# Kernel tuning notes

Hardware: AMD Instinct MI355X
Metric: run time of the kernel (lower is better)

## Reference

```python
import jax, jax.numpy as jnp
import numpy as np

MARGIN = 0.1
NUM_BINS = 1600  # FastAP histogram bins over squared-distance range [0, 4]


def _fastap_rewards(x, labels):
    """Per-query FastAP (Cakir et al.) with soft (triangular) histogram binning.
    x: [n, d] L2-normalized embeddings; labels: [n] int. Returns [n] rewards.
    Uses the fact that a triangular pulse of width delta spreads each distance
    over exactly two adjacent bins -> scatter-add instead of an [n,n,L] tensor."""
    n = x.shape[0]
    L = NUM_BINS + 1
    delta = 4.0 / NUM_BINS
    dist2 = jnp.clip(2.0 - 2.0 * (x @ x.T), 0.0, 4.0)  # [n, n]
    same = labels[:, None] == labels[None, :]
    eye = jnp.eye(n, dtype=bool)
    i_pos = same & ~eye
    i_neg = ~same

    t = dist2 / delta
    idx0 = jnp.clip(jnp.floor(t).astype(jnp.int32), 0, L - 1)
    idx1 = jnp.clip(idx0 + 1, 0, L - 1)
    frac = t - jnp.floor(t)
    rows = jnp.broadcast_to(jnp.arange(n)[:, None], (n, n))

    def hist(mask):
        m = mask.astype(x.dtype)
        h = jnp.zeros((n, L), x.dtype)
        h = h.at[rows, idx0].add((1.0 - frac) * m)
        h = h.at[rows, idx1].add(frac * m)
        return h

    h_pos = hist(i_pos)
    h_neg = hist(i_neg)
    H_pos = jnp.cumsum(h_pos, axis=1)
    H_all = jnp.cumsum(h_pos + h_neg, axis=1)
    n_pos = jnp.sum(i_pos, axis=1).astype(x.dtype)
    safe = H_all > 0
    ap = jnp.sum(jnp.where(safe, h_pos * H_pos / jnp.where(safe, H_all, 1.0), 0.0), axis=1)
    return jnp.where(n_pos > 0, ap / jnp.maximum(n_pos, 1.0), 0.0)


def _per_row_loss(inputs_col, targets_col, inputs_row, targets_row):
    """Vectorized form of compute_loss_list. Sorting in the original only serves
    to extract max pos / max neg similarity, so per-row maxima + masked sums
    reproduce the exact same math."""
    n = inputs_col.shape[0]
    sim = inputs_col @ inputs_row.T  # [n, m]
    pos = targets_col[:, None] == targets_row[None, :]
    neg = ~pos  # computed BEFORE removing the diagonal, as in the original
    eye = jnp.eye(n, dtype=bool)
    pos = pos.at[:, :n].set(pos[:, :n] & ~eye)

    has_pos = jnp.any(pos, axis=1)
    neg_max = jnp.max(jnp.where(neg, sim, -jnp.inf), axis=1)  # neg_pair_[-1]
    pos_max = jnp.max(jnp.where(pos, sim, -jnp.inf), axis=1)  # pos_pair_[-1]

    pos_sel = pos & (sim < (neg_max + MARGIN)[:, None])
    pos_loss = jnp.sum(jnp.where(pos_sel, 1.0 - sim, 0.0), axis=1)

    thr = jnp.maximum(0.6, pos_max) - MARGIN
    neg_sel = neg & (sim > thr[:, None])
    neg_loss = jnp.sum(jnp.where(neg_sel, sim, 0.0), axis=1)

    return jnp.where(has_pos, pos_loss + neg_loss, 0.0), n


def setup_inputs() -> dict:
    key = jax.random.key(0)
    k1, k2, k3, k4, k5 = jax.random.split(key, 5)
    n, m, d, ncls = 4096, 4096, 128, 512

    def unit(k, shape):
        v = jax.random.normal(k, shape, dtype=jnp.float32)
        return v / jnp.linalg.norm(v, axis=-1, keepdims=True)

    return {
        "inputs_col": unit(k1, (n, d)),
        "targets_col": jax.random.randint(k2, (n,), 0, ncls),
        "inputs_row": unit(k3, (m, d)),
        "targets_row": jax.random.randint(k4, (m,), 0, ncls),
        "reward_labels": jax.random.randint(k5, (n,), 0, ncls),
    }


def reference(inputs_col, targets_col, inputs_row, targets_row, reward_labels):
    loss_i, n = _per_row_loss(inputs_col, targets_col, inputs_row, targets_row)
    # torch.tensor(rewards) detaches rewards from the graph -> stop_gradient
    rewards = jax.lax.stop_gradient(_fastap_rewards(inputs_col, reward_labels))
    return jnp.sum(loss_i * (1.0 - rewards)) / n
```

## Files before the change

kernel.cpp:

```cpp
#include <hip/hip_runtime.h>


#define N_ROWS 4096
#define DIM 128
#define TILE 128
#define L_BINS 1601

typedef __bf16 bf16x8 __attribute__((ext_vector_type(8)));
typedef float f32x4 __attribute__((ext_vector_type(4)));

__device__ __forceinline__ unsigned short f32_to_bf16(float f) {
    unsigned int u = __float_as_uint(f);
    u = (u + 0x7FFFu + ((u >> 16) & 1u)) >> 16;
    return (unsigned short)u;
}

__device__ __forceinline__ float bf16_lo(unsigned int u) {
    return __uint_as_float(u << 16);
}
__device__ __forceinline__ float bf16_hi(unsigned int u) {
    return __uint_as_float(u & 0xFFFF0000u);
}

__device__ __forceinline__ void unpack8(uint4 pk, float* s) {
    s[0] = bf16_lo(pk.x); s[1] = bf16_hi(pk.x);
    s[2] = bf16_lo(pk.y); s[3] = bf16_hi(pk.y);
    s[4] = bf16_lo(pk.z); s[5] = bf16_hi(pk.z);
    s[6] = bf16_lo(pk.w); s[7] = bf16_hi(pk.w);
}

__device__ __forceinline__ void async_copy16(const void* g, void* l) {
    __builtin_amdgcn_global_load_lds(
        (const __attribute__((address_space(1))) unsigned int*)g,
        (__attribute__((address_space(3))) unsigned int*)l, 16, 0, 0);
}

__global__ __launch_bounds__(256) void cvt2_kernel(const float4* __restrict__ a,
                                                   const float4* __restrict__ b,
                                                   ushort4* __restrict__ oa,
                                                   ushort4* __restrict__ ob,
                                                   int nvec) {
    for (int idx = blockIdx.x * 256 + threadIdx.x; idx < 2 * nvec; idx += gridDim.x * 256) {
        bool second = idx >= nvec;
        int k = second ? idx - nvec : idx;
        float4 v = second ? b[k] : a[k];
        ushort4 o;
        o.x = f32_to_bf16(v.x); o.y = f32_to_bf16(v.y);
        o.z = f32_to_bf16(v.z); o.w = f32_to_bf16(v.w);
        if (second) ob[k] = o; else oa[k] = o;
    }
}

__global__ __launch_bounds__(256) void gemm_tile_kernel(const unsigned short* __restrict__ A,
                                                        const unsigned short* __restrict__ B0,
                                                        const unsigned short* __restrict__ B1,
                                                        unsigned short* __restrict__ C0,
                                                        unsigned short* __restrict__ C1,
                                                        int N) {
    __shared__ unsigned short As[TILE * DIM];
    __shared__ unsigned short Bs[TILE * DIM];
    int w = threadIdx.x >> 6;
    int lane = threadIdx.x & 63;
    int tm = blockIdx.y, tn = blockIdx.x;
    const unsigned short* B = blockIdx.z ? B1 : B0;
    unsigned short* C = blockIdx.z ? C1 : C0;

    const char* ga = (const char*)(A + (size_t)tm * TILE * DIM);
    const char* gb = (const char*)(B + (size_t)tn * TILE * DIM);
#pragma unroll
    for (int it = 0; it < 8; ++it) {
        int off = (w * 8 + it) * 1024;
        async_copy16(ga + off + lane * 16, (char*)As + off);
        async_copy16(gb + off + lane * 16, (char*)Bs + off);
    }
    __syncthreads();

    int wm = (w & 1) * 64;
    int wn = (w >> 1) * 64;
    int quad = lane >> 4;
    int l15 = lane & 15;

    f32x4 acc[4][4] = {};
#pragma unroll
    for (int kk = 0; kk < 4; ++kk) {
        int kb = kk * 32 + quad * 8;
        bf16x8 af[4], bfr[4];
#pragma unroll
        for (int mi = 0; mi < 4; ++mi)
            af[mi] = *(const bf16x8*)&As[(wm + mi * 16 + l15) * DIM + kb];
#pragma unroll
        for (int ni = 0; ni < 4; ++ni)
            bfr[ni] = *(const bf16x8*)&Bs[(wn + ni * 16 + l15) * DIM + kb];
#pragma unroll
        for (int mi = 0; mi < 4; ++mi)
#pragma unroll
            for (int ni = 0; ni < 4; ++ni)
                acc[mi][ni] = __builtin_amdgcn_mfma_f32_16x16x32_bf16(af[mi], bfr[ni], acc[mi][ni], 0, 0, 0);
    }

#pragma unroll
    for (int mi = 0; mi < 4; ++mi) {
        int row0 = tm * TILE + wm + mi * 16 + quad * 4;
#pragma unroll
        for (int ni = 0; ni < 4; ++ni) {
            int col = tn * TILE + wn + ni * 16 + l15;
#pragma unroll
            for (int r = 0; r < 4; ++r)
                C[(size_t)(row0 + r) * N + col] = f32_to_bf16(acc[mi][ni][r]);
        }
    }
}

__global__ __launch_bounds__(256) void loss_kernel(const unsigned short* __restrict__ sim,
                                                   const int* __restrict__ tcol,
                                                   const int* __restrict__ trow,
                                                   float* __restrict__ loss,
                                                   int n, int m) {
    int i = (blockIdx.x * 256 + threadIdx.x) >> 6;
    int lane = threadIdx.x & 63;
    int myt = tcol[i];

    const uint4* simv = (const uint4*)(sim + (size_t)i * m);
    const int4* labv = (const int4*)trow;

    uint4 pk[8];
    unsigned long long posm = 0ull, negm = 0ull;
    float pmax = -3e38f, nmax = -3e38f;
#pragma unroll
    for (int v = 0; v < 8; ++v) {
        int vi = v * 64 + lane;
        pk[v] = simv[vi];
        int4 l0 = labv[2 * vi];
        int4 l1 = labv[2 * vi + 1];
        int j0 = vi * 8;
        float s[8];
        unpack8(pk[v], s);
        int lab[8] = {l0.x, l0.y, l0.z, l0.w, l1.x, l1.y, l1.z, l1.w};
#pragma unroll
        for (int k = 0; k < 8; ++k) {
            int j = j0 + k;
            bool same = (lab[k] == myt);
            bool posf = same && (j != i);
            if (posf) pmax = fmaxf(pmax, s[k]);
            if (!same) nmax = fmaxf(nmax, s[k]);
            posm |= ((unsigned long long)posf) << (v * 8 + k);
            negm |= ((unsigned long long)(!same)) << (v * 8 + k);
        }
    }
#pragma unroll
    for (int off = 32; off > 0; off >>= 1) {
        pmax = fmaxf(pmax, __shfl_xor(pmax, off));
        nmax = fmaxf(nmax, __shfl_xor(nmax, off));
    }

    float thr_n = nmax + 0.1f;
    float thr_p = fmaxf(0.6f, pmax) - 0.1f;
    float pl = 0.f, nl = 0.f;
#pragma unroll
    for (int v = 0; v < 8; ++v) {
        float s[8];
        unpack8(pk[v], s);
#pragma unroll
        for (int k = 0; k < 8; ++k) {
            int bit = v * 8 + k;
            bool posf = (posm >> bit) & 1ull;
            bool negf = (negm >> bit) & 1ull;
            pl += (posf && s[k] < thr_n) ? 1.f - s[k] : 0.f;
            nl += (negf && s[k] > thr_p) ? s[k] : 0.f;
        }
    }
    float tot = pl + nl;
#pragma unroll
    for (int off = 32; off > 0; off >>= 1) tot += __shfl_xor(tot, off);
    if (lane == 0) loss[i] = (pmax > -1e30f) ? tot : 0.f;
}

__global__ __launch_bounds__(256) void fastap_kernel(const unsigned short* __restrict__ gram,
                                                     const int* __restrict__ labels,
                                                     float* __restrict__ reward,
                                                     int n) {
    __shared__ unsigned long long hist[L_BINS];
    __shared__ unsigned long long wsum[4];
    __shared__ float apw[4];
    __shared__ int npw[4];
    int i = blockIdx.x;
    int t = threadIdx.x;
    int w = t >> 6;
    int lane = t & 63;

    for (int b = t; b < L_BINS; b += 256) hist[b] = 0ull;
    __syncthreads();

    int li = labels[i];
    int npos = 0;
    const uint4* gv = (const uint4*)(gram + (size_t)i * n);
    const int4* labv = (const int4*)labels;

    for (int v = t; v < (n >> 3); v += 256) {
        uint4 pk = gv[v];
        int4 l0 = labv[2 * v];
        int4 l1 = labv[2 * v + 1];
        int j0 = v << 3;
        float s[8];
        unpack8(pk, s);
        int lab[8] = {l0.x, l0.y, l0.z, l0.w, l1.x, l1.y, l1.z, l1.w};
#pragma unroll
        for (int k = 0; k < 8; ++k) {
            int j = j0 + k;
            float d2 = fminf(fmaxf(2.f - 2.f * s[k], 0.f), 4.f);
            float tt = d2 * 400.0f;
            float fl = floorf(tt);
            int i0 = (int)fl;
            if (i0 > L_BINS - 1) i0 = L_BINS - 1;
            int i1 = i0 + 1;
            if (i1 > L_BINS - 1) i1 = L_BINS - 1;
            unsigned int w1 = (unsigned int)((tt - fl) * 65536.0f);
            unsigned int w0 = 65536u - w1;
            bool diag = (j == i);
            if (diag) { w0 = 0u; w1 = 0u; }
            bool posf = (lab[k] == li) && !diag;
            unsigned long long hi = posf ? 1ull : 0ull;
            atomicAdd(&hist[i0], (unsigned long long)w0 | ((hi * w0) << 32));
            atomicAdd(&hist[i1], (unsigned long long)w1 | ((hi * w1) << 32));
            npos += posf ? 1 : 0;
        }
    }
    __syncthreads();

    const int CH = 7;
    int base = t * CH;
    unsigned long long lc[CH];
    unsigned long long run = 0ull;
#pragma unroll
    for (int k = 0; k < CH; ++k) {
        int idx = base + k;
        unsigned long long h = (idx < L_BINS) ? hist[idx] : 0ull;
        run += h;
        lc[k] = run;
    }
    unsigned long long tsum = run;
    unsigned long long sc = tsum;
#pragma unroll
    for (int off = 1; off < 64; off <<= 1) {
        unsigned long long v2 = __shfl_up(sc, off);
        if (lane >= off) sc += v2;
    }
    if (lane == 63) wsum[w] = sc;
    __syncthreads();
    unsigned long long woff = 0ull;
    for (int ww = 0; ww < w; ++ww) woff += wsum[ww];
    unsigned long long throff = woff + sc - tsum;

    float ap = 0.f;
#pragma unroll
    for (int k = 0; k < CH; ++k) {
        int idx = base + k;
        if (idx < L_BINS) {
            unsigned long long h = hist[idx];
            unsigned int hp = (unsigned int)(h >> 32);
            if (hp) {
                unsigned long long cum = lc[k] + throff;
                unsigned int Hp = (unsigned int)(cum >> 32);
                unsigned int Ha = (unsigned int)cum;
                ap += (float)hp * (float)Hp / (float)Ha;
            }
        }
    }
#pragma unroll
    for (int off = 32; off > 0; off >>= 1) {
        ap += __shfl_xor(ap, off);
        npos += __shfl_xor(npos, off);
    }
    if (lane == 0) { apw[w] = ap; npw[w] = npos; }
    __syncthreads();
    if (t == 0) {
        float A = apw[0] + apw[1] + apw[2] + apw[3];
        int np = npw[0] + npw[1] + npw[2] + npw[3];
        reward[i] = (np > 0) ? A * (1.0f / 65536.0f) / (float)np : 0.f;
    }
}

__global__ __launch_bounds__(256) void final_kernel(const float* __restrict__ loss,
                                                    const float* __restrict__ reward,
                                                    float* __restrict__ out, int n) {
    __shared__ float r[256];
    int t = threadIdx.x;
    float s = 0.f;
    for (int j = t; j < n; j += 256) s += loss[j] * (1.f - reward[j]);
    r[t] = s;
    __syncthreads();
    for (int off = 128; off > 0; off >>= 1) {
        if (t < off) r[t] += r[t + off];
        __syncthreads();
    }
    if (t == 0) out[0] = r[0] / (float)n;
}

extern "C" void kernel_launch(void* const* d_in, const int* in_sizes, int n_in,
                              void* d_out, int out_size, void* d_ws, size_t ws_size,
                              hipStream_t stream) {
    const float* inputs_col = (const float*)d_in[0];
    const int* targets_col = (const int*)d_in[1];
    const float* inputs_row = (const float*)d_in[2];
    const int* targets_row = (const int*)d_in[3];
    const int* reward_labels = (const int*)d_in[4];
    float* out = (float*)d_out;

    const int n = N_ROWS, m = N_ROWS, d = DIM;
    char* ws = (char*)d_ws;
    const size_t MB = 1048576;
    unsigned short* simbuf = (unsigned short*)ws;
    unsigned short* grambuf = (unsigned short*)(ws + 32 * MB);
    unsigned short* Abf = (unsigned short*)(ws + 64 * MB);
    unsigned short* Rbf = (unsigned short*)(ws + 65 * MB);
    float* loss = (float*)(ws + 66 * MB);
    float* reward = loss + n;

    cvt2_kernel<<<512, 256, 0, stream>>>((const float4*)inputs_col, (const float4*)inputs_row,
                                         (ushort4*)Abf, (ushort4*)Rbf, n * d / 4);

    dim3 ggrid(n / TILE, n / TILE, 2);
    gemm_tile_kernel<<<ggrid, 256, 0, stream>>>(Abf, Rbf, Abf, simbuf, grambuf, m);

    loss_kernel<<<n / 4, 256, 0, stream>>>(simbuf, targets_col, targets_row, loss, n, m);

    fastap_kernel<<<n, 256, 0, stream>>>(grambuf, reward_labels, reward, n);

    final_kernel<<<1, 256, 0, stream>>>(loss, reward, out, n);
}
```

Before: 136.4 us.

## Fuse per-row loss and FastAP histogram kernels into one block-per-row kernel

```diff
diff --git a/kernel.cpp b/kernel.cpp
--- a/kernel.cpp
+++ b/kernel.cpp
@@ -111,102 +111,76 @@
     }
 }
 
-__global__ __launch_bounds__(256) void loss_kernel(const unsigned short* __restrict__ sim,
-                                                   const int* __restrict__ tcol,
-                                                   const int* __restrict__ trow,
-                                                   float* __restrict__ loss,
-                                                   int n, int m) {
-    int i = (blockIdx.x * 256 + threadIdx.x) >> 6;
-    int lane = threadIdx.x & 63;
+__global__ __launch_bounds__(256) void lossap_kernel(const unsigned short* __restrict__ sim,
+                                                     const unsigned short* __restrict__ gram,
+                                                     const int* __restrict__ tcol,
+                                                     const int* __restrict__ trow,
+                                                     const int* __restrict__ rlab,
+                                                     float* __restrict__ contrib,
+                                                     int n) {
+    __shared__ unsigned long long hist[L_BINS];
+    __shared__ unsigned long long wsum[4];
+    __shared__ float pmx[4], nmx[4], lsum[4], apw[4];
+    __shared__ int npw[4];
+    int i = blockIdx.x;
+    int t = threadIdx.x;
+    int w = t >> 6, lane = t & 63;
+
+    for (int b = t; b < L_BINS; b += 256) hist[b] = 0ull;
+
     int myt = tcol[i];
-
-    const uint4* simv = (const uint4*)(sim + (size_t)i * m);
-    const int4* labv = (const int4*)trow;
-
-    uint4 pk[8];
-    unsigned long long posm = 0ull, negm = 0ull;
+    int li = rlab[i];
+    const uint4* simv = (const uint4*)(sim + (size_t)i * n);
+    const uint4* grav = (const uint4*)(gram + (size_t)i * n);
+    const int4* trv = (const int4*)trow;
+    const int4* rlv = (const int4*)rlab;
+
+    uint4 spk[2], gpk[2];
+    int4 tl[4], rl[4];
+#pragma unroll
+    for (int vv = 0; vv < 2; ++vv) {
+        int vi = vv * 256 + t;
+        spk[vv] = simv[vi];
+        gpk[vv] = grav[vi];
+        tl[2 * vv] = trv[2 * vi];
+        tl[2 * vv + 1] = trv[2 * vi + 1];
+        rl[2 * vv] = rlv[2 * vi];
+        rl[2 * vv + 1] = rlv[2 * vi + 1];
+    }
+
     float pmax = -3e38f, nmax = -3e38f;
-#pragma unroll
-    for (int v = 0; v < 8; ++v) {
-        int vi = v * 64 + lane;
-        pk[v] = simv[vi];
-        int4 l0 = labv[2 * vi];
-        int4 l1 = labv[2 * vi + 1];
-        int j0 = vi * 8;
+    unsigned int posm = 0, negm = 0;
+#pragma unroll
+    for (int vv = 0; vv < 2; ++vv) {
+        int vi = vv * 256 + t;
         float s[8];
-        unpack8(pk[v], s);
-        int lab[8] = {l0.x, l0.y, l0.z, l0.w, l1.x, l1.y, l1.z, l1.w};
+        unpack8(spk[vv], s);
+        int lab[8] = {tl[2 * vv].x, tl[2 * vv].y, tl[2 * vv].z, tl[2 * vv].w,
+                      tl[2 * vv + 1].x, tl[2 * vv + 1].y, tl[2 * vv + 1].z, tl[2 * vv + 1].w};
 #pragma unroll
         for (int k = 0; k < 8; ++k) {
-            int j = j0 + k;
+            int j = vi * 8 + k;
             bool same = (lab[k] == myt);
             bool posf = same && (j != i);
             if (posf) pmax = fmaxf(pmax, s[k]);
             if (!same) nmax = fmaxf(nmax, s[k]);
-            posm |= ((unsigned long long)posf) << (v * 8 + k);
-            negm |= ((unsigned long long)(!same)) << (v * 8 + k);
-        }
-    }
-#pragma unroll
-    for (int off = 32; off > 0; off >>= 1) {
-        pmax = fmaxf(pmax, __shfl_xor(pmax, off));
-        nmax = fmaxf(nmax, __shfl_xor(nmax, off));
-    }
-
-    float thr_n = nmax + 0.1f;
-    float thr_p = fmaxf(0.6f, pmax) - 0.1f;
-    float pl = 0.f, nl = 0.f;
-#pragma unroll
-    for (int v = 0; v < 8; ++v) {
+            posm |= ((unsigned int)posf) << (vv * 8 + k);
+            negm |= ((unsigned int)(!same)) << (vv * 8 + k);
+        }
+    }
+    __syncthreads();
+
+    int npos = 0;
+#pragma unroll
+    for (int vv = 0; vv < 2; ++vv) {
+        int vi = vv * 256 + t;
         float s[8];
-        unpack8(pk[v], s);
+        unpack8(gpk[vv], s);
+        int lab[8] = {rl[2 * vv].x, rl[2 * vv].y, rl[2 * vv].z, rl[2 * vv].w,
+                      rl[2 * vv + 1].x, rl[2 * vv + 1].y, rl[2 * vv + 1].z, rl[2 * vv + 1].w};
 #pragma unroll
         for (int k = 0; k < 8; ++k) {
-            int bit = v * 8 + k;
-            bool posf = (posm >> bit) & 1ull;
-            bool negf = (negm >> bit) & 1ull;
-            pl += (posf && s[k] < thr_n) ? 1.f - s[k] : 0.f;
-            nl += (negf && s[k] > thr_p) ? s[k] : 0.f;
-        }
-    }
-    float tot = pl + nl;
-#pragma unroll
-    for (int off = 32; off > 0; off >>= 1) tot += __shfl_xor(tot, off);
-    if (lane == 0) loss[i] = (pmax > -1e30f) ? tot : 0.f;
-}
-
-__global__ __launch_bounds__(256) void fastap_kernel(const unsigned short* __restrict__ gram,
-                                                     const int* __restrict__ labels,
-                                                     float* __restrict__ reward,
-                                                     int n) {
-    __shared__ unsigned long long hist[L_BINS];
-    __shared__ unsigned long long wsum[4];
-    __shared__ float apw[4];
-    __shared__ int npw[4];
-    int i = blockIdx.x;
-    int t = threadIdx.x;
-    int w = t >> 6;
-    int lane = t & 63;
-
-    for (int b = t; b < L_BINS; b += 256) hist[b] = 0ull;
-    __syncthreads();
-
-    int li = labels[i];
-    int npos = 0;
-    const uint4* gv = (const uint4*)(gram + (size_t)i * n);
-    const int4* labv = (const int4*)labels;
-
-    for (int v = t; v < (n >> 3); v += 256) {
-        uint4 pk = gv[v];
-        int4 l0 = labv[2 * v];
-        int4 l1 = labv[2 * v + 1];
-        int j0 = v << 3;
-        float s[8];
-        unpack8(pk, s);
-        int lab[8] = {l0.x, l0.y, l0.z, l0.w, l1.x, l1.y, l1.z, l1.w};
-#pragma unroll
-        for (int k = 0; k < 8; ++k) {
-            int j = j0 + k;
+            int j = vi * 8 + k;
             float d2 = fminf(fmaxf(2.f - 2.f * s[k], 0.f), 4.f);
             float tt = d2 * 400.0f;
             float fl = floorf(tt);
@@ -225,7 +199,37 @@
             npos += posf ? 1 : 0;
         }
     }
-    __syncthreads();
+
+#pragma unroll
+    for (int off = 32; off > 0; off >>= 1) {
+        pmax = fmaxf(pmax, __shfl_xor(pmax, off));
+        nmax = fmaxf(nmax, __shfl_xor(nmax, off));
+    }
+    if (lane == 0) { pmx[w] = pmax; nmx[w] = nmax; }
+    __syncthreads();
+
+    pmax = fmaxf(fmaxf(pmx[0], pmx[1]), fmaxf(pmx[2], pmx[3]));
+    nmax = fmaxf(fmaxf(nmx[0], nmx[1]), fmaxf(nmx[2], nmx[3]));
+
+    float thr_n = nmax + 0.1f;
+    float thr_p = fmaxf(0.6f, pmax) - 0.1f;
+    float pl = 0.f, nl = 0.f;
+#pragma unroll
+    for (int vv = 0; vv < 2; ++vv) {
+        float s[8];
+        unpack8(spk[vv], s);
+#pragma unroll
+        for (int k = 0; k < 8; ++k) {
+            int bit = vv * 8 + k;
+            bool posf = (posm >> bit) & 1u;
+            bool negf = (negm >> bit) & 1u;
+            pl += (posf && s[k] < thr_n) ? 1.f - s[k] : 0.f;
+            nl += (negf && s[k] > thr_p) ? s[k] : 0.f;
+        }
+    }
+    float tot = pl + nl;
+#pragma unroll
+    for (int off = 32; off > 0; off >>= 1) tot += __shfl_xor(tot, off);
 
     const int CH = 7;
     int base = t * CH;
@@ -246,6 +250,7 @@
         if (lane >= off) sc += v2;
     }
     if (lane == 63) wsum[w] = sc;
+    if (lane == 0) lsum[w] = tot;
     __syncthreads();
     unsigned long long woff = 0ull;
     for (int ww = 0; ww < w; ++ww) woff += wsum[ww];
@@ -274,19 +279,20 @@
     if (lane == 0) { apw[w] = ap; npw[w] = npos; }
     __syncthreads();
     if (t == 0) {
+        float loss_i = (pmax > -1e30f) ? (lsum[0] + lsum[1] + lsum[2] + lsum[3]) : 0.f;
         float A = apw[0] + apw[1] + apw[2] + apw[3];
         int np = npw[0] + npw[1] + npw[2] + npw[3];
-        reward[i] = (np > 0) ? A * (1.0f / 65536.0f) / (float)np : 0.f;
-    }
-}
-
-__global__ __launch_bounds__(256) void final_kernel(const float* __restrict__ loss,
-                                                    const float* __restrict__ reward,
+        float reward = (np > 0) ? A * (1.0f / 65536.0f) / (float)np : 0.f;
+        contrib[i] = loss_i * (1.f - reward);
+    }
+}
+
+__global__ __launch_bounds__(256) void final_kernel(const float* __restrict__ contrib,
                                                     float* __restrict__ out, int n) {
     __shared__ float r[256];
     int t = threadIdx.x;
     float s = 0.f;
-    for (int j = t; j < n; j += 256) s += loss[j] * (1.f - reward[j]);
+    for (int j = t; j < n; j += 256) s += contrib[j];
     r[t] = s;
     __syncthreads();
     for (int off = 128; off > 0; off >>= 1) {
@@ -313,8 +319,7 @@
     unsigned short* grambuf = (unsigned short*)(ws + 32 * MB);
     unsigned short* Abf = (unsigned short*)(ws + 64 * MB);
     unsigned short* Rbf = (unsigned short*)(ws + 65 * MB);
-    float* loss = (float*)(ws + 66 * MB);
-    float* reward = loss + n;
+    float* contrib = (float*)(ws + 66 * MB);
 
     cvt2_kernel<<<512, 256, 0, stream>>>((const float4*)inputs_col, (const float4*)inputs_row,
                                          (ushort4*)Abf, (ushort4*)Rbf, n * d / 4);
@@ -322,9 +327,8 @@
     dim3 ggrid(n / TILE, n / TILE, 2);
     gemm_tile_kernel<<<ggrid, 256, 0, stream>>>(Abf, Rbf, Abf, simbuf, grambuf, m);
 
-    loss_kernel<<<n / 4, 256, 0, stream>>>(simbuf, targets_col, targets_row, loss, n, m);
-
-    fastap_kernel<<<n, 256, 0, stream>>>(grambuf, reward_labels, reward, n);
-
-    final_kernel<<<1, 256, 0, stream>>>(loss, reward, out, n);
-}
+    lossap_kernel<<<n, 256, 0, stream>>>(simbuf, grambuf, targets_col, targets_row,
+                                         reward_labels, contrib, n);
+
+    final_kernel<<<1, 256, 0, stream>>>(contrib, out, n);
+}
```

Result: faster. 126.7 us (-7.1%).
